# Optimization experiments

Hardware: AMD Instinct MI355X
Metric: run time of the kernel (lower is better)

## Reference

```python
import jax, jax.numpy as jnp
import numpy as np

N_NODES = 100000
N_EDGES = 3200000
N_FEATS = 128
HIDDEN = 64
N_GRAPHS = 64


def _uniform(key, shape, fan_in):
    s = 1.0 / np.sqrt(fan_in)
    return jax.random.uniform(key, shape, jnp.float32, -s, s)


def setup_inputs() -> dict:
    key = jax.random.key(0)
    ks = jax.random.split(key, 12)
    x = jax.random.normal(ks[0], (N_NODES, N_FEATS), jnp.float32)
    edge_index = jax.random.randint(ks[1], (2, N_EDGES), 0, N_NODES, dtype=jnp.int32)
    batch = jnp.sort(jax.random.randint(ks[2], (N_NODES,), 0, N_GRAPHS, dtype=jnp.int32))
    return {
        "x": x,
        "edge_index": edge_index,
        "batch": batch,
        "W1": _uniform(ks[3], (N_FEATS, HIDDEN), N_FEATS),
        "b1": jnp.zeros((HIDDEN,), jnp.float32),
        "W2": _uniform(ks[4], (HIDDEN, HIDDEN), HIDDEN),
        "b2": jnp.zeros((HIDDEN,), jnp.float32),
        "W3": _uniform(ks[5], (HIDDEN, HIDDEN), HIDDEN),
        "b3": jnp.zeros((HIDDEN,), jnp.float32),
        "Wl": _uniform(ks[6], (HIDDEN, 1), HIDDEN),
        "bl": jnp.zeros((1,), jnp.float32),
    }


def _gcn_conv(x, W, b, src, dst):
    """PyG GCNConv: add self-loops, symmetric deg^-1/2 normalization, scatter-add."""
    n = x.shape[0]
    h = x @ W                                   # [N, H] transform first (small H)
    loop = jnp.arange(n, dtype=src.dtype)       # self-loops
    s = jnp.concatenate([src, loop])
    d = jnp.concatenate([dst, loop])
    deg = jax.ops.segment_sum(jnp.ones_like(d, dtype=h.dtype), d, num_segments=n)
    dinv = jnp.where(deg > 0, jax.lax.rsqrt(deg), 0.0)
    norm = (dinv[s] * dinv[d])[:, None]         # [E+N, 1]
    out = jax.ops.segment_sum(h[s] * norm, d, num_segments=n)
    return out + b


def reference(x, edge_index, batch, W1, b1, W2, b2, W3, b3, Wl, bl):
    src, dst = edge_index[0], edge_index[1]
    h = jax.nn.relu(_gcn_conv(x, W1, b1, src, dst))
    # dropout p=0.2 is identity at inference (training=False)
    h = jax.nn.relu(_gcn_conv(h, W2, b2, src, dst))
    h = jax.nn.relu(_gcn_conv(h, W3, b3, src, dst))
    # global mean pool over graph ids
    sums = jax.ops.segment_sum(h, batch, num_segments=N_GRAPHS)
    cnt = jax.ops.segment_sum(jnp.ones((h.shape[0],), h.dtype), batch, num_segments=N_GRAPHS)
    pooled = sums / jnp.maximum(cnt, 1.0)[:, None]   # [G, H]
    return pooled @ Wl + bl                          # [G, 1]
```

## Files before the change

kernel.cpp:

```cpp
#include <hip/hip_runtime.h>
#include <hip/hip_fp16.h>

#define NNODES 100000
#define NEDGES 3200000
#define NFEATS 128
#define HID 64
#define NGRAPHS 64
#define NPB 128
#define NBUCK ((NNODES + NPB - 1) / NPB)
#define NBLKA 128
#define EPB (NEDGES / NBLKA)


__global__ __launch_bounds__(256) void k_init(float* pooled, float* gcnt) {
    int i = blockIdx.x * 256 + threadIdx.x;
    if (i < NGRAPHS * HID) pooled[i] = 0.f;
    if (i < NGRAPHS) gcnt[i] = 0.f;
}

__global__ __launch_bounds__(256) void k_hist(const int* __restrict__ dst, int* __restrict__ cntmat) {
    __shared__ int h[NBUCK];
    for (int j = threadIdx.x; j < NBUCK; j += 256) h[j] = 0;
    __syncthreads();
    int e0 = blockIdx.x * EPB;
    for (int i = threadIdx.x; i < EPB; i += 256) atomicAdd(&h[dst[e0 + i] >> 7], 1);
    __syncthreads();
    for (int j = threadIdx.x; j < NBUCK; j += 256) cntmat[blockIdx.x * NBUCK + j] = h[j];
}

__global__ __launch_bounds__(256) void k_offsA(const int* __restrict__ cntmat, int* __restrict__ tot) {
    int j = blockIdx.x * 256 + threadIdx.x;
    if (j >= NBUCK) return;
    int s = 0;
#pragma unroll 8
    for (int b = 0; b < NBLKA; b++) s += cntmat[b * NBUCK + j];
    tot[j] = s;
}

__global__ __launch_bounds__(64) void k_offsB(const int* __restrict__ tot, int* __restrict__ bbase) {
    int tid = threadIdx.x;
    int run = 0;
    for (int c = 0; c < NBUCK; c += 64) {
        int j = c + tid;
        int own = (j < NBUCK) ? tot[j] : 0;
        int v = own;
        for (int off = 1; off < 64; off <<= 1) {
            int u = __shfl_up(v, off);
            if (tid >= off) v += u;
        }
        if (j < NBUCK) bbase[j] = run + v - own;
        run += __shfl(v, 63);
    }
    if (tid == 0) bbase[NBUCK] = NEDGES;
}

__global__ __launch_bounds__(256) void k_offsC(const int* __restrict__ cntmat, const int* __restrict__ bbase,
                                               int* __restrict__ offmat) {
    int j = blockIdx.x * 256 + threadIdx.x;
    if (j >= NBUCK) return;
    int run = bbase[j];
    for (int b = 0; b < NBLKA; b++) { offmat[b * NBUCK + j] = run; run += cntmat[b * NBUCK + j]; }
}

__global__ __launch_bounds__(256) void k_bin(const int* __restrict__ src, const int* __restrict__ dst,
                                             const int* __restrict__ offmat, int* __restrict__ ebin) {
    __shared__ int cur[NBUCK];
    int b = blockIdx.x;
    for (int j = threadIdx.x; j < NBUCK; j += 256) cur[j] = offmat[b * NBUCK + j];
    __syncthreads();
    int e0 = b * EPB;
    for (int i = threadIdx.x; i < EPB; i += 256) {
        int s = src[e0 + i], d = dst[e0 + i];
        int p = atomicAdd(&cur[d >> 7], 1);
        ebin[p] = s | ((d & (NPB - 1)) << 17);
    }
}

__global__ __launch_bounds__(256) void k_csr(const int* __restrict__ ebin, const int* __restrict__ bbase,
                                             int* __restrict__ cnt, int* __restrict__ rowptr,
                                             float* __restrict__ dinv, int* __restrict__ cols) {
    __shared__ int h[NPB];
    __shared__ int sc[NPB];
    __shared__ int cur[NPB];
    int j = blockIdx.x;
    int tid = threadIdx.x;
    if (tid < NPB) h[tid] = 0;
    __syncthreads();
    int lo = bbase[j], hi = bbase[j + 1];
    for (int i = lo + tid; i < hi; i += 256) atomicAdd(&h[ebin[i] >> 17], 1);
    __syncthreads();
    if (tid < 64) {
        int run = 0;
        for (int c = 0; c < NPB; c += 64) {
            int own = h[c + tid];
            int v = own;
            for (int off = 1; off < 64; off <<= 1) {
                int u = __shfl_up(v, off);
                if (tid >= off) v += u;
            }
            sc[c + tid] = run + v - own;
            run += __shfl(v, 63);
        }
    }
    __syncthreads();
    int node = j * NPB + tid;
    if (tid < NPB) {
        cur[tid] = lo + sc[tid];
        if (node < NNODES) {
            int c = h[tid];
            cnt[node] = c;
            rowptr[node] = lo + sc[tid];
            dinv[node] = rsqrtf((float)(c + 1));
        }
    }
    __syncthreads();
    for (int i = lo + tid; i < hi; i += 256) {
        int r = ebin[i];
        int p = atomicAdd(&cur[r >> 17], 1);
        cols[p] = r & 0x1FFFF;
    }
}


#define CHK 32
#define CHKP 33

template <int K, bool RELU>
__global__ __launch_bounds__(256) void k_mm(const float* __restrict__ in, const float* __restrict__ W,
                                            const float* __restrict__ dinv, __half* __restrict__ t_out) {
    __shared__ float xs[128 * CHKP];
    const int tid = threadIdx.x;
    const int lane = tid & 63;
    const int wid = tid >> 6;
    const int jhalf = __builtin_amdgcn_readfirstlane(wid & 1);
    const int nloc = (wid >> 1) * 64 + lane;
    const int node0 = blockIdx.x * 128;
    const int node = node0 + nloc;

    float acc[32];
#pragma unroll
    for (int j = 0; j < 32; j++) acc[j] = 0.f;

    const int c4 = tid & 7;
    const int r0 = tid >> 3;

    for (int ko = 0; ko < K; ko += CHK) {
        __syncthreads();
#pragma unroll
        for (int s = 0; s < 4; s++) {
            int r = r0 + s * 32;
            int gn = node0 + r;
            float4 v = make_float4(0.f, 0.f, 0.f, 0.f);
            if (gn < NNODES) v = *(const float4*)&in[(size_t)gn * K + c4 * 4 + ko];
            if (RELU) {
                v.x = fmaxf(v.x, 0.f); v.y = fmaxf(v.y, 0.f);
                v.z = fmaxf(v.z, 0.f); v.w = fmaxf(v.w, 0.f);
            }
            float* dp = &xs[r * CHKP + c4 * 4];
            dp[0] = v.x; dp[1] = v.y; dp[2] = v.z; dp[3] = v.w;
        }
        __syncthreads();
        for (int kk = 0; kk < CHK; kk++) {
            float xk = xs[nloc * CHKP + kk];
            const float* Wr = &W[(size_t)(ko + kk) * 64 + jhalf * 32];
#pragma unroll
            for (int j = 0; j < 32; j++) acc[j] = fmaf(xk, Wr[j], acc[j]);
        }
    }

    if (node < NNODES) {
        float dv = dinv[node];
        __half* tp = &t_out[(size_t)node * 64 + jhalf * 32];
#pragma unroll
        for (int j4 = 0; j4 < 8; j4++) {
            union { __half2 h[2]; float2 f; } u;
            u.h[0] = __floats2half2_rn(acc[j4*4] * dv, acc[j4*4+1] * dv);
            u.h[1] = __floats2half2_rn(acc[j4*4+2] * dv, acc[j4*4+3] * dv);
            *(float2*)&tp[j4 * 4] = u.f;
        }
    }
}


__device__ __forceinline__ void agg_edge(const __half* t, int s, int ql, float4& acc) {
    float2 raw = *(const float2*)&t[(size_t)s * 64 + ql * 4];
    const __half2* hp = (const __half2*)&raw;
    float2 f0 = __half22float2(hp[0]);
    float2 f1 = __half22float2(hp[1]);
    acc.x += f0.x; acc.y += f0.y; acc.z += f1.x; acc.w += f1.y;
}

__global__ __launch_bounds__(256) void k_agg(const __half* __restrict__ t, const int* __restrict__ rowptr,
                                             const int* __restrict__ cnt, const int* __restrict__ cols,
                                             const float* __restrict__ dinv, const float* __restrict__ bias,
                                             float* __restrict__ B) {
    int w = (blockIdx.x * 256 + threadIdx.x) >> 6;
    int lane = threadIdx.x & 63;
    if (w >= NNODES) return;
    int qg = lane >> 4;
    int ql = lane & 15;
    int start = rowptr[w];
    int n = cnt[w];
    float4 acc = make_float4(0.f, 0.f, 0.f, 0.f);
    int e = 0;
    for (; e + 16 <= n; e += 16) {
        int s0 = cols[start + e + qg];
        int s1 = cols[start + e + 4 + qg];
        int s2 = cols[start + e + 8 + qg];
        int s3 = cols[start + e + 12 + qg];
        agg_edge(t, s0, ql, acc);
        agg_edge(t, s1, ql, acc);
        agg_edge(t, s2, ql, acc);
        agg_edge(t, s3, ql, acc);
    }
    for (e += qg; e < n; e += 4) {
        agg_edge(t, cols[start + e], ql, acc);
    }
    acc.x += __shfl_xor(acc.x, 16); acc.y += __shfl_xor(acc.y, 16);
    acc.z += __shfl_xor(acc.z, 16); acc.w += __shfl_xor(acc.w, 16);
    acc.x += __shfl_xor(acc.x, 32); acc.y += __shfl_xor(acc.y, 32);
    acc.z += __shfl_xor(acc.z, 32); acc.w += __shfl_xor(acc.w, 32);
    if (qg == 0) {
        float2 raw = *(const float2*)&t[(size_t)w * 64 + ql * 4];
        const __half2* hp = (const __half2*)&raw;
        float2 f0 = __half22float2(hp[0]);
        float2 f1 = __half22float2(hp[1]);
        float dv = dinv[w];
        float4 b4 = *(const float4*)&bias[ql * 4];
        float4 o;
        o.x = fmaf(dv, f0.x + acc.x, b4.x);
        o.y = fmaf(dv, f0.y + acc.y, b4.y);
        o.z = fmaf(dv, f1.x + acc.z, b4.z);
        o.w = fmaf(dv, f1.y + acc.w, b4.w);
        *(float4*)&B[(size_t)w * 64 + ql * 4] = o;
    }
}


#define POOL_CHUNK 32
__global__ __launch_bounds__(256) void k_pool(const float* __restrict__ h, const int* __restrict__ batch,
                                              float* pooled, float* gcnt) {
    int w = (blockIdx.x * 256 + threadIdx.x) >> 6;
    int lane = threadIdx.x & 63;
    int start = w * POOL_CHUNK;
    if (start >= NNODES) return;
    int end = min(start + POOL_CHUNK, NNODES);
    int g = batch[start];
    float acc = 0.f;
    float cn = 0.f;
    int i = start;
    for (; i + 4 <= end; i += 4) {
        int b0 = batch[i], b1 = batch[i + 1], b2 = batch[i + 2], b3 = batch[i + 3];
        float v0 = h[(size_t)i * 64 + lane];
        float v1 = h[(size_t)(i + 1) * 64 + lane];
        float v2 = h[(size_t)(i + 2) * 64 + lane];
        float v3 = h[(size_t)(i + 3) * 64 + lane];
        if (b0 != g) {
            atomicAdd(&pooled[g * 64 + lane], acc);
            if (lane == 0) atomicAdd(&gcnt[g], cn);
            g = b0; acc = 0.f; cn = 0.f;
        }
        acc += fmaxf(v0, 0.f); cn += 1.f;
        if (b1 != g) {
            atomicAdd(&pooled[g * 64 + lane], acc);
            if (lane == 0) atomicAdd(&gcnt[g], cn);
            g = b1; acc = 0.f; cn = 0.f;
        }
        acc += fmaxf(v1, 0.f); cn += 1.f;
        if (b2 != g) {
            atomicAdd(&pooled[g * 64 + lane], acc);
            if (lane == 0) atomicAdd(&gcnt[g], cn);
            g = b2; acc = 0.f; cn = 0.f;
        }
        acc += fmaxf(v2, 0.f); cn += 1.f;
        if (b3 != g) {
            atomicAdd(&pooled[g * 64 + lane], acc);
            if (lane == 0) atomicAdd(&gcnt[g], cn);
            g = b3; acc = 0.f; cn = 0.f;
        }
        acc += fmaxf(v3, 0.f); cn += 1.f;
    }
    for (; i < end; i++) {
        int gi = batch[i];
        if (gi != g) {
            atomicAdd(&pooled[g * 64 + lane], acc);
            if (lane == 0) atomicAdd(&gcnt[g], cn);
            g = gi; acc = 0.f; cn = 0.f;
        }
        acc += fmaxf(h[(size_t)i * 64 + lane], 0.f);
        cn += 1.f;
    }
    atomicAdd(&pooled[g * 64 + lane], acc);
    if (lane == 0) atomicAdd(&gcnt[g], cn);
}

__global__ __launch_bounds__(256) void k_final(const float* __restrict__ pooled, const float* __restrict__ gcnt,
                                               const float* __restrict__ Wl, const float* __restrict__ bl,
                                               float* __restrict__ out) {
    int g = (blockIdx.x * 256 + threadIdx.x) >> 6;
    int lane = threadIdx.x & 63;
    if (g >= NGRAPHS) return;
    float c = fmaxf(gcnt[g], 1.f);
    float v = pooled[g * 64 + lane] / c * Wl[lane];
#pragma unroll
    for (int off = 32; off; off >>= 1) v += __shfl_down(v, off);
    if (lane == 0) out[g] = v + bl[0];
}


extern "C" void kernel_launch(void* const* d_in, const int* in_sizes, int n_in,
                              void* d_out, int out_size, void* d_ws, size_t ws_size,
                              hipStream_t stream) {
    const float* x  = (const float*)d_in[0];
    const int* ei   = (const int*)d_in[1];
    const int* batch = (const int*)d_in[2];
    const float* W1 = (const float*)d_in[3];
    const float* b1 = (const float*)d_in[4];
    const float* W2 = (const float*)d_in[5];
    const float* b2 = (const float*)d_in[6];
    const float* W3 = (const float*)d_in[7];
    const float* b3 = (const float*)d_in[8];
    const float* Wl = (const float*)d_in[9];
    const float* bl = (const float*)d_in[10];
    const int* src = ei;
    const int* dst = ei + NEDGES;

    char* ws = (char*)d_ws;
    size_t off = 0;
    auto alloc = [&](size_t bytes) { void* p = ws + off; off += (bytes + 255) & ~size_t(255); return p; };
    __half* A      = (__half*)alloc((size_t)NNODES * 64 * 2);
    float*  B      = (float*)alloc((size_t)NNODES * 64 * 4);
    int*    cols   = (int*)alloc((size_t)NEDGES * 4);
    float*  dinv   = (float*)alloc((size_t)NNODES * 4);
    int*    cnt    = (int*)alloc((size_t)NNODES * 4);
    int*    rowptr = (int*)alloc((size_t)NNODES * 4);
    int*    cntmat = (int*)alloc((size_t)NBLKA * NBUCK * 4);
    int*    offmat = (int*)alloc((size_t)NBLKA * NBUCK * 4);
    int*    tot    = (int*)alloc(NBUCK * 4);
    int*    bbase  = (int*)alloc((NBUCK + 1) * 4);
    float*  pooled = (float*)alloc(NGRAPHS * 64 * 4);
    float*  gcnt   = (float*)alloc(NGRAPHS * 4);
    float*  out    = (float*)d_out;
    int*    ebin   = (int*)A;

    const int NB_MM = (NNODES + 127) / 128;
    const int NB_W  = ((size_t)NNODES * 64 + 255) / 256;
    const int NB_PL = ((NNODES + POOL_CHUNK - 1) / POOL_CHUNK + 3) / 4;
    const int NB_J  = (NBUCK + 255) / 256;

    k_init<<<(NGRAPHS * HID + 255) / 256, 256, 0, stream>>>(pooled, gcnt);
    k_hist<<<NBLKA, 256, 0, stream>>>(dst, cntmat);
    k_offsA<<<NB_J, 256, 0, stream>>>(cntmat, tot);
    k_offsB<<<1, 64, 0, stream>>>(tot, bbase);
    k_offsC<<<NB_J, 256, 0, stream>>>(cntmat, bbase, offmat);
    k_bin<<<NBLKA, 256, 0, stream>>>(src, dst, offmat, ebin);
    k_csr<<<NBUCK, 256, 0, stream>>>(ebin, bbase, cnt, rowptr, dinv, cols);

    k_mm<128, false><<<NB_MM, 256, 0, stream>>>(x, W1, dinv, A);
    k_agg<<<NB_W, 256, 0, stream>>>(A, rowptr, cnt, cols, dinv, b1, B);
    k_mm<64, true><<<NB_MM, 256, 0, stream>>>(B, W2, dinv, A);
    k_agg<<<NB_W, 256, 0, stream>>>(A, rowptr, cnt, cols, dinv, b2, B);
    k_mm<64, true><<<NB_MM, 256, 0, stream>>>(B, W3, dinv, A);
    k_agg<<<NB_W, 256, 0, stream>>>(A, rowptr, cnt, cols, dinv, b3, B);

    k_pool<<<NB_PL, 256, 0, stream>>>(B, batch, pooled, gcnt);
    k_final<<<(NGRAPHS * 64 + 255) / 256, 256, 0, stream>>>(pooled, gcnt, Wl, bl, out);
}
```

Baseline: 419.3 us.

## Split transformed features into 16-wide slices for cache-local aggregation, store activations in fp16

New measurement: 618.5 us. 1.48x slower.

```diff
diff --git a/kernel.cpp b/kernel.cpp
--- a/kernel.cpp
+++ b/kernel.cpp
@@ -10,13 +10,9 @@
 #define NBUCK ((NNODES + NPB - 1) / NPB)
 #define NBLKA 128
 #define EPB (NEDGES / NBLKA)
-
-
-__global__ __launch_bounds__(256) void k_init(float* pooled, float* gcnt) {
-    int i = blockIdx.x * 256 + threadIdx.x;
-    if (i < NGRAPHS * HID) pooled[i] = 0.f;
-    if (i < NGRAPHS) gcnt[i] = 0.f;
-}
+#define NF4 16
+#define SLICE ((size_t)NNODES * NF4)
+
 
 __global__ __launch_bounds__(256) void k_hist(const int* __restrict__ dst, int* __restrict__ cntmat) {
     __shared__ int h[NBUCK];
@@ -37,29 +33,32 @@
     tot[j] = s;
 }
 
-__global__ __launch_bounds__(64) void k_offsB(const int* __restrict__ tot, int* __restrict__ bbase) {
+__global__ __launch_bounds__(256) void k_offsBC(const int* __restrict__ tot, const int* __restrict__ cntmat,
+                                                int* __restrict__ bbase, int* __restrict__ offmat,
+                                                float* pooled, float* gcnt) {
     int tid = threadIdx.x;
-    int run = 0;
-    for (int c = 0; c < NBUCK; c += 64) {
-        int j = c + tid;
-        int own = (j < NBUCK) ? tot[j] : 0;
-        int v = own;
-        for (int off = 1; off < 64; off <<= 1) {
-            int u = __shfl_up(v, off);
-            if (tid >= off) v += u;
-        }
-        if (j < NBUCK) bbase[j] = run + v - own;
-        run += __shfl(v, 63);
-    }
-    if (tid == 0) bbase[NBUCK] = NEDGES;
-}
-
-__global__ __launch_bounds__(256) void k_offsC(const int* __restrict__ cntmat, const int* __restrict__ bbase,
-                                               int* __restrict__ offmat) {
-    int j = blockIdx.x * 256 + threadIdx.x;
-    if (j >= NBUCK) return;
-    int run = bbase[j];
-    for (int b = 0; b < NBLKA; b++) { offmat[b * NBUCK + j] = run; run += cntmat[b * NBUCK + j]; }
+    if (tid < 64) {
+        int run = 0;
+        for (int c = 0; c < NBUCK; c += 64) {
+            int j = c + tid;
+            int own = (j < NBUCK) ? tot[j] : 0;
+            int v = own;
+            for (int off = 1; off < 64; off <<= 1) {
+                int u = __shfl_up(v, off);
+                if (tid >= off) v += u;
+            }
+            if (j < NBUCK) bbase[j] = run + v - own;
+            run += __shfl(v, 63);
+        }
+        if (tid == 0) bbase[NBUCK] = NEDGES;
+    }
+    for (int i = tid; i < NGRAPHS * HID; i += 256) pooled[i] = 0.f;
+    if (tid < NGRAPHS) gcnt[tid] = 0.f;
+    __syncthreads();
+    for (int j = tid; j < NBUCK; j += 256) {
+        int run = bbase[j];
+        for (int b = 0; b < NBLKA; b++) { offmat[b * NBUCK + j] = run; run += cntmat[b * NBUCK + j]; }
+    }
 }
 
 __global__ __launch_bounds__(256) void k_bin(const int* __restrict__ src, const int* __restrict__ dst,
@@ -122,12 +121,26 @@
 }
 
 
+__device__ __forceinline__ void store_t4(float* acc, float dv, int jhalf, int node, __half* t4) {
+#pragma unroll
+    for (int hh = 0; hh < 2; hh++) {
+        int fg = jhalf * 2 + hh;
+        __half* tp = t4 + (size_t)fg * SLICE + (size_t)node * NF4;
+        union { __half2 h2[8]; float4 f[2]; } u;
+#pragma unroll
+        for (int q = 0; q < 8; q++)
+            u.h2[q] = __floats2half2_rn(acc[hh * 16 + 2 * q] * dv, acc[hh * 16 + 2 * q + 1] * dv);
+        *(float4*)tp = u.f[0];
+        *(float4*)(tp + 8) = u.f[1];
+    }
+}
+
+
 #define CHK 32
 #define CHKP 33
 
-template <int K, bool RELU>
-__global__ __launch_bounds__(256) void k_mm(const float* __restrict__ in, const float* __restrict__ W,
-                                            const float* __restrict__ dinv, __half* __restrict__ t_out) {
+__global__ __launch_bounds__(256) void k_mm128(const float* __restrict__ in, const float* __restrict__ W,
+                                               const float* __restrict__ dinv, __half* __restrict__ t4) {
     __shared__ float xs[128 * CHKP];
     const int tid = threadIdx.x;
     const int lane = tid & 63;
@@ -144,18 +157,14 @@
     const int c4 = tid & 7;
     const int r0 = tid >> 3;
 
-    for (int ko = 0; ko < K; ko += CHK) {
+    for (int ko = 0; ko < 128; ko += CHK) {
         __syncthreads();
 #pragma unroll
         for (int s = 0; s < 4; s++) {
             int r = r0 + s * 32;
             int gn = node0 + r;
             float4 v = make_float4(0.f, 0.f, 0.f, 0.f);
-            if (gn < NNODES) v = *(const float4*)&in[(size_t)gn * K + c4 * 4 + ko];
-            if (RELU) {
-                v.x = fmaxf(v.x, 0.f); v.y = fmaxf(v.y, 0.f);
-                v.z = fmaxf(v.z, 0.f); v.w = fmaxf(v.w, 0.f);
-            }
+            if (gn < NNODES) v = *(const float4*)&in[(size_t)gn * 128 + c4 * 4 + ko];
             float* dp = &xs[r * CHKP + c4 * 4];
             dp[0] = v.x; dp[1] = v.y; dp[2] = v.z; dp[3] = v.w;
         }
@@ -168,77 +177,117 @@
         }
     }
 
-    if (node < NNODES) {
-        float dv = dinv[node];
-        __half* tp = &t_out[(size_t)node * 64 + jhalf * 32];
-#pragma unroll
-        for (int j4 = 0; j4 < 8; j4++) {
-            union { __half2 h[2]; float2 f; } u;
-            u.h[0] = __floats2half2_rn(acc[j4*4] * dv, acc[j4*4+1] * dv);
-            u.h[1] = __floats2half2_rn(acc[j4*4+2] * dv, acc[j4*4+3] * dv);
-            *(float2*)&tp[j4 * 4] = u.f;
-        }
-    }
-}
-
-
-__device__ __forceinline__ void agg_edge(const __half* t, int s, int ql, float4& acc) {
-    float2 raw = *(const float2*)&t[(size_t)s * 64 + ql * 4];
-    const __half2* hp = (const __half2*)&raw;
-    float2 f0 = __half22float2(hp[0]);
-    float2 f1 = __half22float2(hp[1]);
-    acc.x += f0.x; acc.y += f0.y; acc.z += f1.x; acc.w += f1.y;
-}
-
-__global__ __launch_bounds__(256) void k_agg(const __half* __restrict__ t, const int* __restrict__ rowptr,
+    if (node < NNODES) store_t4(acc, dinv[node], jhalf, node, t4);
+}
+
+
+__global__ __launch_bounds__(256) void k_mmh(const __half* __restrict__ in, const float* __restrict__ W,
+                                             const float* __restrict__ dinv, __half* __restrict__ t4) {
+    __shared__ float xs[128 * 65];
+    const int tid = threadIdx.x;
+    const int lane = tid & 63;
+    const int wid = tid >> 6;
+    const int jhalf = __builtin_amdgcn_readfirstlane(wid & 1);
+    const int nloc = (wid >> 1) * 64 + lane;
+    const int node0 = blockIdx.x * 128;
+    const int node = node0 + nloc;
+
+    const int c8 = tid & 7;
+    const int r0 = tid >> 3;
+#pragma unroll
+    for (int s = 0; s < 4; s++) {
+        int r = r0 + s * 32;
+        int gn = node0 + r;
+        float4 raw = make_float4(0.f, 0.f, 0.f, 0.f);
+        if (gn < NNODES) raw = *(const float4*)&in[(size_t)gn * 64 + c8 * 8];
+        const __half2* hp = (const __half2*)&raw;
+        float* dp = &xs[r * 65 + c8 * 8];
+#pragma unroll
+        for (int q = 0; q < 4; q++) {
+            float2 f = __half22float2(hp[q]);
+            dp[2 * q] = f.x; dp[2 * q + 1] = f.y;
+        }
+    }
+    __syncthreads();
+
+    float acc[32];
+#pragma unroll
+    for (int j = 0; j < 32; j++) acc[j] = 0.f;
+    for (int kk = 0; kk < 64; kk++) {
+        float xk = xs[nloc * 65 + kk];
+        const float* Wr = &W[(size_t)kk * 64 + jhalf * 32];
+#pragma unroll
+        for (int j = 0; j < 32; j++) acc[j] = fmaf(xk, Wr[j], acc[j]);
+    }
+
+    if (node < NNODES) store_t4(acc, dinv[node], jhalf, node, t4);
+}
+
+
+__global__ __launch_bounds__(256) void k_agg(const __half* __restrict__ t4, const int* __restrict__ rowptr,
                                              const int* __restrict__ cnt, const int* __restrict__ cols,
                                              const float* __restrict__ dinv, const float* __restrict__ bias,
-                                             float* __restrict__ B) {
-    int w = (blockIdx.x * 256 + threadIdx.x) >> 6;
+                                             __half* __restrict__ B) {
+    int bid = blockIdx.x;
+    int fg = (bid & 7) >> 1;
+    int ng = (bid >> 3) * 2 + (bid & 1);
+    int w = ng * 4 + (threadIdx.x >> 6);
     int lane = threadIdx.x & 63;
-    if (w >= NNODES) return;
-    int qg = lane >> 4;
-    int ql = lane & 15;
+    int es = lane >> 2;
+    int f = lane & 3;
+    const __half* ts = t4 + (size_t)fg * SLICE;
     int start = rowptr[w];
     int n = cnt[w];
     float4 acc = make_float4(0.f, 0.f, 0.f, 0.f);
-    int e = 0;
-    for (; e + 16 <= n; e += 16) {
-        int s0 = cols[start + e + qg];
-        int s1 = cols[start + e + 4 + qg];
-        int s2 = cols[start + e + 8 + qg];
-        int s3 = cols[start + e + 12 + qg];
-        agg_edge(t, s0, ql, acc);
-        agg_edge(t, s1, ql, acc);
-        agg_edge(t, s2, ql, acc);
-        agg_edge(t, s3, ql, acc);
-    }
-    for (e += qg; e < n; e += 4) {
-        agg_edge(t, cols[start + e], ql, acc);
-    }
+    int e = es;
+    for (; e + 16 < n; e += 32) {
+        int s0 = cols[start + e];
+        int s1 = cols[start + e + 16];
+        float2 r0 = *(const float2*)&ts[(size_t)s0 * NF4 + f * 4];
+        float2 r1 = *(const float2*)&ts[(size_t)s1 * NF4 + f * 4];
+        const __half2* h0 = (const __half2*)&r0;
+        const __half2* h1 = (const __half2*)&r1;
+        float2 a0 = __half22float2(h0[0]), b0 = __half22float2(h0[1]);
+        float2 a1 = __half22float2(h1[0]), b1 = __half22float2(h1[1]);
+        acc.x += a0.x + a1.x; acc.y += a0.y + a1.y;
+        acc.z += b0.x + b1.x; acc.w += b0.y + b1.y;
+    }
+    if (e < n) {
+        int s0 = cols[start + e];
+        float2 r0 = *(const float2*)&ts[(size_t)s0 * NF4 + f * 4];
+        const __half2* h0 = (const __half2*)&r0;
+        float2 a0 = __half22float2(h0[0]), b0 = __half22float2(h0[1]);
+        acc.x += a0.x; acc.y += a0.y; acc.z += b0.x; acc.w += b0.y;
+    }
+    acc.x += __shfl_xor(acc.x, 4);  acc.y += __shfl_xor(acc.y, 4);
+    acc.z += __shfl_xor(acc.z, 4);  acc.w += __shfl_xor(acc.w, 4);
+    acc.x += __shfl_xor(acc.x, 8);  acc.y += __shfl_xor(acc.y, 8);
+    acc.z += __shfl_xor(acc.z, 8);  acc.w += __shfl_xor(acc.w, 8);
     acc.x += __shfl_xor(acc.x, 16); acc.y += __shfl_xor(acc.y, 16);
     acc.z += __shfl_xor(acc.z, 16); acc.w += __shfl_xor(acc.w, 16);
     acc.x += __shfl_xor(acc.x, 32); acc.y += __shfl_xor(acc.y, 32);
     acc.z += __shfl_xor(acc.z, 32); acc.w += __shfl_xor(acc.w, 32);
-    if (qg == 0) {
-        float2 raw = *(const float2*)&t[(size_t)w * 64 + ql * 4];
+    if (es == 0) {
+        float2 raw = *(const float2*)&ts[(size_t)w * NF4 + f * 4];
         const __half2* hp = (const __half2*)&raw;
         float2 f0 = __half22float2(hp[0]);
         float2 f1 = __half22float2(hp[1]);
         float dv = dinv[w];
-        float4 b4 = *(const float4*)&bias[ql * 4];
-        float4 o;
-        o.x = fmaf(dv, f0.x + acc.x, b4.x);
-        o.y = fmaf(dv, f0.y + acc.y, b4.y);
-        o.z = fmaf(dv, f1.x + acc.z, b4.z);
-        o.w = fmaf(dv, f1.y + acc.w, b4.w);
-        *(float4*)&B[(size_t)w * 64 + ql * 4] = o;
+        float4 b4 = *(const float4*)&bias[fg * NF4 + f * 4];
+        float ox = fmaxf(fmaf(dv, f0.x + acc.x, b4.x), 0.f);
+        float oy = fmaxf(fmaf(dv, f0.y + acc.y, b4.y), 0.f);
+        float oz = fmaxf(fmaf(dv, f1.x + acc.z, b4.z), 0.f);
+        float ow = fmaxf(fmaf(dv, f1.y + acc.w, b4.w), 0.f);
+        union { __half2 h2[2]; float2 ff; } u;
+        u.h2[0] = __floats2half2_rn(ox, oy);
+        u.h2[1] = __floats2half2_rn(oz, ow);
+        *(float2*)&B[(size_t)w * 64 + fg * NF4 + f * 4] = u.ff;
     }
 }
 
 
 #define POOL_CHUNK 32
-__global__ __launch_bounds__(256) void k_pool(const float* __restrict__ h, const int* __restrict__ batch,
+__global__ __launch_bounds__(256) void k_pool(const __half* __restrict__ h, const int* __restrict__ batch,
                                               float* pooled, float* gcnt) {
     int w = (blockIdx.x * 256 + threadIdx.x) >> 6;
     int lane = threadIdx.x & 63;
@@ -251,34 +300,34 @@
     int i = start;
     for (; i + 4 <= end; i += 4) {
         int b0 = batch[i], b1 = batch[i + 1], b2 = batch[i + 2], b3 = batch[i + 3];
-        float v0 = h[(size_t)i * 64 + lane];
-        float v1 = h[(size_t)(i + 1) * 64 + lane];
-        float v2 = h[(size_t)(i + 2) * 64 + lane];
-        float v3 = h[(size_t)(i + 3) * 64 + lane];
+        float v0 = __half2float(h[(size_t)i * 64 + lane]);
+        float v1 = __half2float(h[(size_t)(i + 1) * 64 + lane]);
+        float v2 = __half2float(h[(size_t)(i + 2) * 64 + lane]);
+        float v3 = __half2float(h[(size_t)(i + 3) * 64 + lane]);
         if (b0 != g) {
             atomicAdd(&pooled[g * 64 + lane], acc);
             if (lane == 0) atomicAdd(&gcnt[g], cn);
             g = b0; acc = 0.f; cn = 0.f;
         }
-        acc += fmaxf(v0, 0.f); cn += 1.f;
+        acc += v0; cn += 1.f;
         if (b1 != g) {
             atomicAdd(&pooled[g * 64 + lane], acc);
             if (lane == 0) atomicAdd(&gcnt[g], cn);
             g = b1; acc = 0.f; cn = 0.f;
         }
-        acc += fmaxf(v1, 0.f); cn += 1.f;
+        acc += v1; cn += 1.f;
         if (b2 != g) {
             atomicAdd(&pooled[g * 64 + lane], acc);
             if (lane == 0) atomicAdd(&gcnt[g], cn);
             g = b2; acc = 0.f; cn = 0.f;
         }
-        acc += fmaxf(v2, 0.f); cn += 1.f;
+        acc += v2; cn += 1.f;
         if (b3 != g) {
             atomicAdd(&pooled[g * 64 + lane], acc);
             if (lane == 0) atomicAdd(&gcnt[g], cn);
             g = b3; acc = 0.f; cn = 0.f;
         }
-        acc += fmaxf(v3, 0.f); cn += 1.f;
+        acc += v3; cn += 1.f;
     }
     for (; i < end; i++) {
         int gi = batch[i];
@@ -287,7 +336,7 @@
             if (lane == 0) atomicAdd(&gcnt[g], cn);
             g = gi; acc = 0.f; cn = 0.f;
         }
-        acc += fmaxf(h[(size_t)i * 64 + lane], 0.f);
+        acc += __half2float(h[(size_t)i * 64 + lane]);
         cn += 1.f;
     }
     atomicAdd(&pooled[g * 64 + lane], acc);
@@ -328,8 +377,8 @@
     char* ws = (char*)d_ws;
     size_t off = 0;
     auto alloc = [&](size_t bytes) { void* p = ws + off; off += (bytes + 255) & ~size_t(255); return p; };
-    __half* A      = (__half*)alloc((size_t)NNODES * 64 * 2);
-    float*  B      = (float*)alloc((size_t)NNODES * 64 * 4);
+    __half* t4     = (__half*)alloc((size_t)NNODES * 64 * 2);
+    __half* B      = (__half*)alloc((size_t)NNODES * 64 * 2);
     int*    cols   = (int*)alloc((size_t)NEDGES * 4);
     float*  dinv   = (float*)alloc((size_t)NNODES * 4);
     int*    cnt    = (int*)alloc((size_t)NNODES * 4);
@@ -341,27 +390,25 @@
     float*  pooled = (float*)alloc(NGRAPHS * 64 * 4);
     float*  gcnt   = (float*)alloc(NGRAPHS * 4);
     float*  out    = (float*)d_out;
-    int*    ebin   = (int*)A;
+    int*    ebin   = (int*)t4;
 
     const int NB_MM = (NNODES + 127) / 128;
-    const int NB_W  = ((size_t)NNODES * 64 + 255) / 256;
+    const int NB_AG = (NNODES / 4 / 2) * 8;
     const int NB_PL = ((NNODES + POOL_CHUNK - 1) / POOL_CHUNK + 3) / 4;
     const int NB_J  = (NBUCK + 255) / 256;
 
-    k_init<<<(NGRAPHS * HID + 255) / 256, 256, 0, stream>>>(pooled, gcnt);
     k_hist<<<NBLKA, 256, 0, stream>>>(dst, cntmat);
     k_offsA<<<NB_J, 256, 0, stream>>>(cntmat, tot);
-    k_offsB<<<1, 64, 0, stream>>>(tot, bbase);
-    k_offsC<<<NB_J, 256, 0, stream>>>(cntmat, bbase, offmat);
+    k_offsBC<<<1, 256, 0, stream>>>(tot, cntmat, bbase, offmat, pooled, gcnt);
     k_bin<<<NBLKA, 256, 0, stream>>>(src, dst, offmat, ebin);
     k_csr<<<NBUCK, 256, 0, stream>>>(ebin, bbase, cnt, rowptr, dinv, cols);
 
-    k_mm<128, false><<<NB_MM, 256, 0, stream>>>(x, W1, dinv, A);
-    k_agg<<<NB_W, 256, 0, stream>>>(A, rowptr, cnt, cols, dinv, b1, B);
-    k_mm<64, true><<<NB_MM, 256, 0, stream>>>(B, W2, dinv, A);
-    k_agg<<<NB_W, 256, 0, stream>>>(A, rowptr, cnt, cols, dinv, b2, B);
-    k_mm<64, true><<<NB_MM, 256, 0, stream>>>(B, W3, dinv, A);
-    k_agg<<<NB_W, 256, 0, stream>>>(A, rowptr, cnt, cols, dinv, b3, B);
+    k_mm128<<<NB_MM, 256, 0, stream>>>(x, W1, dinv, t4);
+    k_agg<<<NB_AG, 256, 0, stream>>>(t4, rowptr, cnt, cols, dinv, b1, B);
+    k_mmh<<<NB_MM, 256, 0, stream>>>(B, W2, dinv, t4);
+    k_agg<<<NB_AG, 256, 0, stream>>>(t4, rowptr, cnt, cols, dinv, b2, B);
+    k_mmh<<<NB_MM, 256, 0, stream>>>(B, W3, dinv, t4);
+    k_agg<<<NB_AG, 256, 0, stream>>>(t4, rowptr, cnt, cols, dinv, b3, B);
 
     k_pool<<<NB_PL, 256, 0, stream>>>(B, batch, pooled, gcnt);
     k_final<<<(NGRAPHS * 64 + 255) / 256, 256, 0, stream>>>(pooled, gcnt, Wl, bl, out);
```
